# Performance work log

Hardware: AMD Instinct MI355X
Metric: run time of the kernel (lower is better)

Reference implementation:

```python
import jax, jax.numpy as jnp
import numpy as np

WINDOW = 7
NUM_HEADS = 12

def _relative_position_index(ws: int) -> np.ndarray:
    coords = np.stack(np.meshgrid(np.arange(ws), np.arange(ws), indexing='ij'))  # (2, ws, ws)
    flat = coords.reshape(2, -1)  # (2, N)
    rel = flat[:, :, None] - flat[:, None, :]  # (2, N, N)
    rel = rel.transpose(1, 2, 0).copy()
    rel[:, :, 0] += ws - 1
    rel[:, :, 1] += ws - 1
    rel[:, :, 0] *= 2 * ws - 1
    return rel.sum(-1)  # (N, N) int

REL_IDX = jnp.asarray(_relative_position_index(WINDOW))  # (49, 49)

def setup_inputs() -> dict:
    key = jax.random.key(0)
    ks = jax.random.split(key, 7)
    B_, N, C = 2048, 49, 384
    nW = 64
    return {
        'x': jax.random.normal(ks[0], (B_, N, C), jnp.float32),
        'mask': jax.random.normal(ks[1], (nW, N, N), jnp.float32),
        'qkv_w': jax.random.normal(ks[2], (3 * C, C), jnp.float32) * 0.02,
        'qkv_b': jax.random.normal(ks[3], (3 * C,), jnp.float32) * 0.02,
        'proj_w': jax.random.normal(ks[4], (C, C), jnp.float32) * 0.02,
        'proj_b': jax.random.normal(ks[5], (C,), jnp.float32) * 0.02,
        'rel_bias_table': jax.random.normal(ks[6], ((2 * WINDOW - 1) ** 2, NUM_HEADS), jnp.float32) * 0.02,
    }

def reference(x, mask, qkv_w, qkv_b, proj_w, proj_b, rel_bias_table):
    B_, N, C = x.shape
    H = NUM_HEADS
    D = C // H
    scale = D ** -0.5
    # fused qkv projection: (B_, N, 3C) -> (3, B_, H, N, D)
    qkv = (x @ qkv_w.T + qkv_b).reshape(B_, N, 3, H, D).transpose(2, 0, 3, 1, 4)
    q, k, v = qkv[0], qkv[1], qkv[2]
    attn = jnp.einsum('bhnd,bhmd->bhnm', q, k) * scale  # (B_, H, N, N)
    # relative position bias gather: (N, N, H) -> (H, N, N)
    bias = rel_bias_table[REL_IDX].transpose(2, 0, 1)
    attn = attn + bias[None]
    nW = mask.shape[0]
    B = B_ // nW
    attn = attn.reshape(B, nW, H, N, N) + mask[None, :, None]
    attn = attn.reshape(B_, H, N, N)
    attn = jax.nn.softmax(attn, axis=-1)
    out = jnp.einsum('bhnm,bhmd->bnhd', attn, v).reshape(B_, N, C)
    return out @ proj_w.T + proj_b
```

## Files before the change

kernel.cpp:

```cpp
#include <hip/hip_runtime.h>
#include <hip/hip_bf16.h>
#include <stdint.h>
#include <stddef.h>

typedef __attribute__((ext_vector_type(8))) short short8;
typedef __attribute__((ext_vector_type(4))) float floatx4;

#define GLDS16(gptr, lptr)                                                         \
  __builtin_amdgcn_global_load_lds(                                                \
      (const __attribute__((address_space(1))) void*)(gptr),                       \
      (__attribute__((address_space(3))) void*)(lptr), 16, 0, 0)

#define MTOT  100352
#define KDIM  384
#define NQKV  1152
#define NPROJ 384

__global__ void cvt_kernel(const float* __restrict__ in,
                           __hip_bfloat16* __restrict__ out, int n4) {
    int i = blockIdx.x * blockDim.x + threadIdx.x;
    if (i >= n4) return;
    float4 v = ((const float4*)in)[i];
    __hip_bfloat16* o = out + (size_t)i * 4;
    o[0] = __float2bfloat16(v.x);
    o[1] = __float2bfloat16(v.y);
    o[2] = __float2bfloat16(v.z);
    o[3] = __float2bfloat16(v.w);
}

__global__ void build_bias_kernel(const float* __restrict__ tbl,
                                  const float* __restrict__ mask,
                                  float* __restrict__ combined) {
    int tid = blockIdx.x * 256 + threadIdx.x;
    if (tid >= 12 * 64 * 2401) return;
    int hw = tid / 2401;
    int nm = tid - hw * 2401;
    int h  = hw / 64;
    int w2 = hw - h * 64;
    int n = nm / 49;
    int m = nm - n * 49;
    int i1 = n / 7, j1 = n - i1 * 7;
    int i2 = m / 7, j2 = m - i2 * 7;
    int ridx = (i1 - i2 + 6) * 13 + (j1 - j2 + 6);
    combined[tid] = tbl[ridx * 12 + h] + mask[(size_t)w2 * 2401 + nm];
}

template <int EPI>
__global__ __launch_bounds__(256) void gemm_bt_kernel(
    const __hip_bfloat16* __restrict__ A, const __hip_bfloat16* __restrict__ B,
    const float* __restrict__ bias, float* __restrict__ Cout,
    __hip_bfloat16* __restrict__ qbuf, __hip_bfloat16* __restrict__ kbuf,
    __hip_bfloat16* __restrict__ vbuf, int N) {
    __shared__ __hip_bfloat16 sA[128 * 32];
    __shared__ __hip_bfloat16 sB[128 * 32];
    const int t = threadIdx.x;
    const int bm = blockIdx.x, bn = blockIdx.y;
    const int lane = t & 63;
    const int w = t >> 6;
    const int wm = w & 1, wn = w >> 1;
    const int quad = lane >> 4, l15 = lane & 15;
    const int srow = t >> 2;
    const int scol = (t & 3) << 3;

    const __hip_bfloat16* Ab = A + (size_t)bm * 128 * KDIM;
    const __hip_bfloat16* Bb = B + (size_t)bn * 128 * KDIM;

    const floatx4 fzero = {0.f, 0.f, 0.f, 0.f};
    floatx4 acc[4][4];
#pragma unroll
    for (int i = 0; i < 4; ++i)
#pragma unroll
        for (int j = 0; j < 4; ++j) acc[i][j] = fzero;

    for (int kk = 0; kk < KDIM; kk += 32) {
        GLDS16(Ab + (size_t)srow * KDIM + kk + scol, &sA[srow * 32 + scol]);
        GLDS16(Ab + (size_t)(srow + 64) * KDIM + kk + scol,
               &sA[(srow + 64) * 32 + scol]);
        GLDS16(Bb + (size_t)srow * KDIM + kk + scol, &sB[srow * 32 + scol]);
        GLDS16(Bb + (size_t)(srow + 64) * KDIM + kk + scol,
               &sB[(srow + 64) * 32 + scol]);
        __syncthreads();
        short8 af[4], bf[4];
#pragma unroll
        for (int i = 0; i < 4; ++i)
            af[i] = *(const short8*)&sA[(wm * 64 + i * 16 + l15) * 32 + quad * 8];
#pragma unroll
        for (int j = 0; j < 4; ++j)
            bf[j] = *(const short8*)&sB[(wn * 64 + j * 16 + l15) * 32 + quad * 8];
#pragma unroll
        for (int i = 0; i < 4; ++i)
#pragma unroll
            for (int j = 0; j < 4; ++j)
                acc[i][j] = __builtin_amdgcn_mfma_f32_16x16x32_bf16(
                    af[i], bf[j], acc[i][j], 0, 0, 0);
        __syncthreads();
    }

    if (EPI == 0) {
        const float scale = 0.17677669529663687f;
#pragma unroll
        for (int j = 0; j < 4; ++j) {
            const int col = bn * 128 + wn * 64 + j * 16 + l15;
            const int part = col / 384;
            const int within = col - part * 384;
            const int hh = within >> 5;
            const int d = within & 31;
            __hip_bfloat16* dst = (part == 0) ? qbuf : ((part == 1) ? kbuf : vbuf);
            const float bv = bias[col];
            const float mul = (part == 0) ? scale : 1.0f;
#pragma unroll
            for (int i = 0; i < 4; ++i) {
#pragma unroll
                for (int r = 0; r < 4; ++r) {
                    const int row = bm * 128 + wm * 64 + i * 16 + quad * 4 + r;
                    const int b = row / 49;
                    const int nn = row - b * 49;
                    const float val = (acc[i][j][r] + bv) * mul;
                    dst[(((size_t)b * 12 + hh) * 49 + nn) * 32 + d] =
                        __float2bfloat16(val);
                }
            }
        }
    } else {
#pragma unroll
        for (int j = 0; j < 4; ++j) {
            const int col = bn * 128 + wn * 64 + j * 16 + l15;
            const float bv = bias[col];
#pragma unroll
            for (int i = 0; i < 4; ++i) {
#pragma unroll
                for (int r = 0; r < 4; ++r) {
                    const int row = bm * 128 + wm * 64 + i * 16 + quad * 4 + r;
                    Cout[(size_t)row * N + col] = acc[i][j][r] + bv;
                }
            }
        }
    }
}

__global__ __launch_bounds__(64) void attn_kernel(
    const __hip_bfloat16* __restrict__ qbuf,
    const __hip_bfloat16* __restrict__ kbuf,
    const __hip_bfloat16* __restrict__ vbuf,
    const float* __restrict__ combined,
    __hip_bfloat16* __restrict__ attn_out) {
    __shared__ __hip_bfloat16 sP[64 * 64];
    const int id = blockIdx.x;
    const int h = id % 12;
    const int b_ = id / 12;
    const int wdx = b_ & 63;
    const int lane = threadIdx.x;
    const int quad = lane >> 4, l15 = lane & 15;
    const size_t base = (size_t)(b_ * 12 + h) * (49 * 32);
    const short* qb = (const short*)qbuf + base;
    const short* kb = (const short*)kbuf + base;
    const short* vb = (const short*)vbuf + base;

    const floatx4 fzero = {0.f, 0.f, 0.f, 0.f};

    short8 aQ[4], bK[4];
#pragma unroll
    for (int i = 0; i < 4; ++i) {
        int r = i * 16 + l15;
        r = r > 48 ? 48 : r;
        aQ[i] = *(const short8*)(qb + r * 32 + quad * 8);
    }
#pragma unroll
    for (int j = 0; j < 4; ++j) {
        int n = j * 16 + l15;
        n = n > 48 ? 48 : n;
        bK[j] = *(const short8*)(kb + n * 32 + quad * 8);
    }

    floatx4 S[4][4];
#pragma unroll
    for (int i = 0; i < 4; ++i)
#pragma unroll
        for (int j = 0; j < 4; ++j)
            S[i][j] =
                __builtin_amdgcn_mfma_f32_16x16x32_bf16(aQ[i], bK[j], fzero, 0, 0, 0);

    const float* cb = combined + (size_t)(h * 64 + wdx) * 2401;
#pragma unroll
    for (int i = 0; i < 4; ++i) {
#pragma unroll
        for (int r = 0; r < 4; ++r) {
            const int row = i * 16 + quad * 4 + r;
            float v0[4];
#pragma unroll
            for (int j = 0; j < 4; ++j) {
                const int col = j * 16 + l15;
                float s = S[i][j][r];
                if (row < 49 && col < 49)
                    s += cb[row * 49 + col];
                else
                    s = -1e30f;
                v0[j] = s;
            }
            float mx = fmaxf(fmaxf(v0[0], v0[1]), fmaxf(v0[2], v0[3]));
#pragma unroll
            for (int off = 8; off > 0; off >>= 1) mx = fmaxf(mx, __shfl_xor(mx, off));
            float sum = 0.f;
#pragma unroll
            for (int j = 0; j < 4; ++j) {
                v0[j] = __expf(v0[j] - mx);
                sum += v0[j];
            }
#pragma unroll
            for (int off = 8; off > 0; off >>= 1) sum += __shfl_xor(sum, off);
            const float inv = 1.0f / sum;
#pragma unroll
            for (int j = 0; j < 4; ++j)
                sP[row * 64 + j * 16 + l15] = __float2bfloat16(v0[j] * inv);
        }
    }
    __syncthreads();

    short8 aP[4][2];
#pragma unroll
    for (int i = 0; i < 4; ++i)
#pragma unroll
        for (int kk = 0; kk < 2; ++kk)
            aP[i][kk] =
                *(const short8*)&sP[(i * 16 + l15) * 64 + kk * 32 + quad * 8];

    short8 bV[2][2];
#pragma unroll
    for (int jd = 0; jd < 2; ++jd)
#pragma unroll
        for (int kk = 0; kk < 2; ++kk) {
            short8 tmp;
#pragma unroll
            for (int jj = 0; jj < 8; ++jj) {
                int k = kk * 32 + quad * 8 + jj;
                k = k > 48 ? 48 : k;
                tmp[jj] = vb[k * 32 + jd * 16 + l15];
            }
            bV[jd][kk] = tmp;
        }

    floatx4 O[4][2];
#pragma unroll
    for (int i = 0; i < 4; ++i)
#pragma unroll
        for (int jd = 0; jd < 2; ++jd) {
            floatx4 o = __builtin_amdgcn_mfma_f32_16x16x32_bf16(aP[i][0], bV[jd][0],
                                                                fzero, 0, 0, 0);
            o = __builtin_amdgcn_mfma_f32_16x16x32_bf16(aP[i][1], bV[jd][1], o, 0, 0,
                                                        0);
            O[i][jd] = o;
        }

#pragma unroll
    for (int i = 0; i < 4; ++i) {
#pragma unroll
        for (int r = 0; r < 4; ++r) {
            const int row = i * 16 + quad * 4 + r;
            if (row < 49) {
#pragma unroll
                for (int jd = 0; jd < 2; ++jd) {
                    attn_out[((size_t)b_ * 49 + row) * 384 + h * 32 + jd * 16 + l15] =
                        __float2bfloat16(O[i][jd][r]);
                }
            }
        }
    }
}

extern "C" void kernel_launch(void* const* d_in, const int* in_sizes, int n_in,
                              void* d_out, int out_size, void* d_ws,
                              size_t ws_size, hipStream_t stream) {
    (void)in_sizes; (void)n_in; (void)out_size; (void)ws_size;
    const float* x      = (const float*)d_in[0];
    const float* mask   = (const float*)d_in[1];
    const float* qkv_w  = (const float*)d_in[2];
    const float* qkv_b  = (const float*)d_in[3];
    const float* proj_w = (const float*)d_in[4];
    const float* proj_b = (const float*)d_in[5];
    const float* tbl    = (const float*)d_in[6];
    float* out = (float*)d_out;
    char* ws = (char*)d_ws;

    __hip_bfloat16* x_bf    = (__hip_bfloat16*)(ws);
    __hip_bfloat16* wq_bf   = (__hip_bfloat16*)(ws + 77070336);
    __hip_bfloat16* wp_bf   = (__hip_bfloat16*)(ws + 77955072);
    float*          combined = (float*)(ws + 78249984);
    __hip_bfloat16* q_buf   = (__hip_bfloat16*)(ws + 85625856);
    __hip_bfloat16* k_buf   = (__hip_bfloat16*)(ws + 162696192);
    __hip_bfloat16* v_buf   = (__hip_bfloat16*)(ws + 239766528);
    __hip_bfloat16* attn_out = x_bf;

    cvt_kernel<<<(MTOT * KDIM / 4 + 255) / 256, 256, 0, stream>>>(x, x_bf,
                                                                  MTOT * KDIM / 4);
    cvt_kernel<<<(NQKV * KDIM / 4 + 255) / 256, 256, 0, stream>>>(
        qkv_w, wq_bf, NQKV * KDIM / 4);
    cvt_kernel<<<(NPROJ * KDIM / 4 + 255) / 256, 256, 0, stream>>>(
        proj_w, wp_bf, NPROJ * KDIM / 4);
    build_bias_kernel<<<(12 * 64 * 2401 + 255) / 256, 256, 0, stream>>>(tbl, mask,
                                                                        combined);
    gemm_bt_kernel<0><<<dim3(MTOT / 128, NQKV / 128), 256, 0, stream>>>(
        x_bf, wq_bf, qkv_b, nullptr, q_buf, k_buf, v_buf, NQKV);
    attn_kernel<<<2048 * 12, 64, 0, stream>>>(q_buf, k_buf, v_buf, combined,
                                              attn_out);
    gemm_bt_kernel<1><<<dim3(MTOT / 128, NPROJ / 128), 256, 0, stream>>>(
        attn_out, wp_bf, proj_b, out, nullptr, nullptr, nullptr, NPROJ);
}
```

Measured before the change: 657.8 us.

## Deepen GEMM K-tile with swizzled LDS, remap grid, transpose S and V layout in attention

The GEMM K-step grows from 32 to 64, LDS gets an XOR swizzle against bank conflicts, blocks are remapped into chunks of 16 M-tiles per N column for L2 reuse, and launch bounds request 4 blocks per CU. The attention kernel computes S transposed so each lane owns a row, reads a padded 52-wide bias with float4 loads, and cuts softmax shuffles to two per row. When the workspace is large enough, V is stored transposed so B fragments load as one vector instead of eight scalar gathers. Block order is changed to h-major, and the bias buffer now reuses the qkv weight region, so it is built after the QKV GEMM.

```diff
diff --git a/kernel.cpp b/kernel.cpp
--- a/kernel.cpp
+++ b/kernel.cpp
@@ -15,6 +15,11 @@
 #define KDIM  384
 #define NQKV  1152
 #define NPROJ 384
+
+static __device__ __forceinline__ unsigned short bfu(float f) {
+    __hip_bfloat16 h = __float2bfloat16(f);
+    return *(unsigned short*)&h;
+}
 
 __global__ void cvt_kernel(const float* __restrict__ in,
                            __hip_bfloat16* __restrict__ out, int n4) {
@@ -30,37 +35,48 @@
 
 __global__ void build_bias_kernel(const float* __restrict__ tbl,
                                   const float* __restrict__ mask,
-                                  float* __restrict__ combined) {
+                                  float* __restrict__ comb) {
     int tid = blockIdx.x * 256 + threadIdx.x;
-    if (tid >= 12 * 64 * 2401) return;
-    int hw = tid / 2401;
-    int nm = tid - hw * 2401;
-    int h  = hw / 64;
-    int w2 = hw - h * 64;
-    int n = nm / 49;
-    int m = nm - n * 49;
-    int i1 = n / 7, j1 = n - i1 * 7;
-    int i2 = m / 7, j2 = m - i2 * 7;
-    int ridx = (i1 - i2 + 6) * 13 + (j1 - j2 + 6);
-    combined[tid] = tbl[ridx * 12 + h] + mask[(size_t)w2 * 2401 + nm];
+    if (tid >= 12 * 64 * 49 * 52) return;
+    int hw = tid / 2548;
+    int nm = tid - hw * 2548;
+    int row = nm / 52;
+    int col = nm - row * 52;
+    int h = hw >> 6;
+    int w2 = hw & 63;
+    float v = -1e30f;
+    if (col < 49) {
+        int i1 = row / 7, j1 = row - i1 * 7;
+        int i2 = col / 7, j2 = col - i2 * 7;
+        int ridx = (i1 - i2 + 6) * 13 + (j1 - j2 + 6);
+        v = tbl[ridx * 12 + h] + mask[(size_t)w2 * 2401 + row * 49 + col];
+    }
+    comb[tid] = v;
 }
 
 template <int EPI>
-__global__ __launch_bounds__(256) void gemm_bt_kernel(
+__global__ __launch_bounds__(256, 4) void gemm_bt_kernel(
     const __hip_bfloat16* __restrict__ A, const __hip_bfloat16* __restrict__ B,
     const float* __restrict__ bias, float* __restrict__ Cout,
     __hip_bfloat16* __restrict__ qbuf, __hip_bfloat16* __restrict__ kbuf,
-    __hip_bfloat16* __restrict__ vbuf, int N) {
-    __shared__ __hip_bfloat16 sA[128 * 32];
-    __shared__ __hip_bfloat16 sB[128 * 32];
+    __hip_bfloat16* __restrict__ vbuf, int N, int NBN, int vt_mode) {
+    __shared__ __hip_bfloat16 sA[128 * 64];
+    __shared__ __hip_bfloat16 sB[128 * 64];
     const int t = threadIdx.x;
-    const int bm = blockIdx.x, bn = blockIdx.y;
+    const int per_chunk = 16 * NBN;
+    const int chunk = blockIdx.x / per_chunk;
+    const int rr = blockIdx.x - chunk * per_chunk;
+    const int bn = rr >> 4;
+    const int bm = chunk * 16 + (rr & 15);
+
     const int lane = t & 63;
     const int w = t >> 6;
     const int wm = w & 1, wn = w >> 1;
     const int quad = lane >> 4, l15 = lane & 15;
-    const int srow = t >> 2;
-    const int scol = (t & 3) << 3;
+    const int srow = t >> 3;
+    const int scg = t & 7;
+    const int sg = scg ^ (srow & 7);
+    const int rsw = l15 & 7;
 
     const __hip_bfloat16* Ab = A + (size_t)bm * 128 * KDIM;
     const __hip_bfloat16* Bb = B + (size_t)bn * 128 * KDIM;
@@ -72,196 +88,241 @@
 #pragma unroll
         for (int j = 0; j < 4; ++j) acc[i][j] = fzero;
 
-    for (int kk = 0; kk < KDIM; kk += 32) {
-        GLDS16(Ab + (size_t)srow * KDIM + kk + scol, &sA[srow * 32 + scol]);
-        GLDS16(Ab + (size_t)(srow + 64) * KDIM + kk + scol,
-               &sA[(srow + 64) * 32 + scol]);
-        GLDS16(Bb + (size_t)srow * KDIM + kk + scol, &sB[srow * 32 + scol]);
-        GLDS16(Bb + (size_t)(srow + 64) * KDIM + kk + scol,
-               &sB[(srow + 64) * 32 + scol]);
+    for (int kk = 0; kk < KDIM; kk += 64) {
+#pragma unroll
+        for (int i = 0; i < 4; ++i) {
+            const int r0 = srow + i * 32;
+            GLDS16(Ab + (size_t)r0 * KDIM + kk + sg * 8, &sA[r0 * 64 + scg * 8]);
+            GLDS16(Bb + (size_t)r0 * KDIM + kk + sg * 8, &sB[r0 * 64 + scg * 8]);
+        }
         __syncthreads();
-        short8 af[4], bf[4];
-#pragma unroll
-        for (int i = 0; i < 4; ++i)
-            af[i] = *(const short8*)&sA[(wm * 64 + i * 16 + l15) * 32 + quad * 8];
-#pragma unroll
-        for (int j = 0; j < 4; ++j)
-            bf[j] = *(const short8*)&sB[(wn * 64 + j * 16 + l15) * 32 + quad * 8];
-#pragma unroll
-        for (int i = 0; i < 4; ++i)
+#pragma unroll
+        for (int kk2 = 0; kk2 < 2; ++kk2) {
+            short8 af[4], bf[4];
+#pragma unroll
+            for (int i = 0; i < 4; ++i)
+                af[i] = *(const short8*)&sA[(wm * 64 + i * 16 + l15) * 64 +
+                                            ((kk2 * 4 + quad) ^ rsw) * 8];
 #pragma unroll
             for (int j = 0; j < 4; ++j)
-                acc[i][j] = __builtin_amdgcn_mfma_f32_16x16x32_bf16(
-                    af[i], bf[j], acc[i][j], 0, 0, 0);
+                bf[j] = *(const short8*)&sB[(wn * 64 + j * 16 + l15) * 64 +
+                                            ((kk2 * 4 + quad) ^ rsw) * 8];
+#pragma unroll
+            for (int i = 0; i < 4; ++i)
+#pragma unroll
+                for (int j = 0; j < 4; ++j)
+                    acc[i][j] = __builtin_amdgcn_mfma_f32_16x16x32_bf16(
+                        af[i], bf[j], acc[i][j], 0, 0, 0);
+        }
         __syncthreads();
+    }
+
+    int colv[4];
+    float bv4[4];
+#pragma unroll
+    for (int j = 0; j < 4; ++j) {
+        colv[j] = bn * 128 + wn * 64 + j * 16 + l15;
+        bv4[j] = bias[colv[j]];
     }
 
     if (EPI == 0) {
         const float scale = 0.17677669529663687f;
+        int partv[4], hv4[4], dv4[4];
 #pragma unroll
         for (int j = 0; j < 4; ++j) {
-            const int col = bn * 128 + wn * 64 + j * 16 + l15;
-            const int part = col / 384;
-            const int within = col - part * 384;
-            const int hh = within >> 5;
-            const int d = within & 31;
-            __hip_bfloat16* dst = (part == 0) ? qbuf : ((part == 1) ? kbuf : vbuf);
-            const float bv = bias[col];
-            const float mul = (part == 0) ? scale : 1.0f;
-#pragma unroll
-            for (int i = 0; i < 4; ++i) {
-#pragma unroll
-                for (int r = 0; r < 4; ++r) {
-                    const int row = bm * 128 + wm * 64 + i * 16 + quad * 4 + r;
-                    const int b = row / 49;
-                    const int nn = row - b * 49;
-                    const float val = (acc[i][j][r] + bv) * mul;
-                    dst[(((size_t)b * 12 + hh) * 49 + nn) * 32 + d] =
-                        __float2bfloat16(val);
+            partv[j] = colv[j] >= 768 ? 2 : (colv[j] >= 384 ? 1 : 0);
+            int within = colv[j] - partv[j] * 384;
+            hv4[j] = within >> 5;
+            dv4[j] = within & 31;
+        }
+#pragma unroll
+        for (int i = 0; i < 4; ++i) {
+#pragma unroll
+            for (int r = 0; r < 4; ++r) {
+                const int row = bm * 128 + wm * 64 + i * 16 + quad * 4 + r;
+                const int b = row / 49;
+                const int nn = row - b * 49;
+#pragma unroll
+                for (int j = 0; j < 4; ++j) {
+                    const float val = acc[i][j][r] + bv4[j];
+                    const size_t bh = (size_t)b * 12 + hv4[j];
+                    if (partv[j] == 0)
+                        qbuf[(bh * 49 + nn) * 32 + dv4[j]] =
+                            __float2bfloat16(val * scale);
+                    else if (partv[j] == 1)
+                        kbuf[(bh * 49 + nn) * 32 + dv4[j]] = __float2bfloat16(val);
+                    else {
+                        if (vt_mode)
+                            vbuf[(bh * 32 + dv4[j]) * 56 + nn] = __float2bfloat16(val);
+                        else
+                            vbuf[(bh * 49 + nn) * 32 + dv4[j]] = __float2bfloat16(val);
+                    }
                 }
             }
         }
     } else {
 #pragma unroll
-        for (int j = 0; j < 4; ++j) {
-            const int col = bn * 128 + wn * 64 + j * 16 + l15;
-            const float bv = bias[col];
-#pragma unroll
-            for (int i = 0; i < 4; ++i) {
-#pragma unroll
-                for (int r = 0; r < 4; ++r) {
-                    const int row = bm * 128 + wm * 64 + i * 16 + quad * 4 + r;
-                    Cout[(size_t)row * N + col] = acc[i][j][r] + bv;
-                }
-            }
-        }
-    }
-}
-
+        for (int i = 0; i < 4; ++i) {
+#pragma unroll
+            for (int r = 0; r < 4; ++r) {
+                const int row = bm * 128 + wm * 64 + i * 16 + quad * 4 + r;
+#pragma unroll
+                for (int j = 0; j < 4; ++j)
+                    Cout[(size_t)row * N + colv[j]] = acc[i][j][r] + bv4[j];
+            }
+        }
+    }
+}
+
+template <int VT>
 __global__ __launch_bounds__(64) void attn_kernel(
     const __hip_bfloat16* __restrict__ qbuf,
     const __hip_bfloat16* __restrict__ kbuf,
-    const __hip_bfloat16* __restrict__ vbuf,
-    const float* __restrict__ combined,
+    const __hip_bfloat16* __restrict__ vslab,
+    const float* __restrict__ comb,
     __hip_bfloat16* __restrict__ attn_out) {
-    __shared__ __hip_bfloat16 sP[64 * 64];
+    __shared__ unsigned short sP[64 * 72];
     const int id = blockIdx.x;
-    const int h = id % 12;
-    const int b_ = id / 12;
-    const int wdx = b_ & 63;
+    const int h = id >> 11;
+    const int rem = id & 2047;
+    const int w = rem >> 5;
+    const int b = rem & 31;
+    const int b_ = b * 64 + w;
     const int lane = threadIdx.x;
     const int quad = lane >> 4, l15 = lane & 15;
-    const size_t base = (size_t)(b_ * 12 + h) * (49 * 32);
-    const short* qb = (const short*)qbuf + base;
-    const short* kb = (const short*)kbuf + base;
-    const short* vb = (const short*)vbuf + base;
+    const size_t bh = (size_t)b_ * 12 + h;
+    const short* qb = (const short*)qbuf + bh * 1568;
+    const short* kb = (const short*)kbuf + bh * 1568;
+    const short* vb = (const short*)vslab + bh * (VT ? 1792 : 1568);
 
     const floatx4 fzero = {0.f, 0.f, 0.f, 0.f};
 
-    short8 aQ[4], bK[4];
-#pragma unroll
-    for (int i = 0; i < 4; ++i) {
-        int r = i * 16 + l15;
-        r = r > 48 ? 48 : r;
-        aQ[i] = *(const short8*)(qb + r * 32 + quad * 8);
-    }
-#pragma unroll
-    for (int j = 0; j < 4; ++j) {
-        int n = j * 16 + l15;
+    short8 bQ[4], aK[4];
+#pragma unroll
+    for (int im = 0; im < 4; ++im) {
+        int m = im * 16 + l15;
+        m = m > 48 ? 48 : m;
+        bQ[im] = *(const short8*)(qb + m * 32 + quad * 8);
+    }
+#pragma unroll
+    for (int jn = 0; jn < 4; ++jn) {
+        int n = jn * 16 + l15;
         n = n > 48 ? 48 : n;
-        bK[j] = *(const short8*)(kb + n * 32 + quad * 8);
-    }
-
-    floatx4 S[4][4];
-#pragma unroll
-    for (int i = 0; i < 4; ++i)
-#pragma unroll
-        for (int j = 0; j < 4; ++j)
-            S[i][j] =
-                __builtin_amdgcn_mfma_f32_16x16x32_bf16(aQ[i], bK[j], fzero, 0, 0, 0);
-
-    const float* cb = combined + (size_t)(h * 64 + wdx) * 2401;
-#pragma unroll
-    for (int i = 0; i < 4; ++i) {
+        aK[jn] = *(const short8*)(kb + n * 32 + quad * 8);
+    }
+
+    floatx4 ST[4][4];
+#pragma unroll
+    for (int im = 0; im < 4; ++im)
+#pragma unroll
+        for (int jn = 0; jn < 4; ++jn)
+            ST[im][jn] = __builtin_amdgcn_mfma_f32_16x16x32_bf16(aK[jn], bQ[im],
+                                                                 fzero, 0, 0, 0);
+
+    const float* cb = comb + (size_t)(h * 64 + w) * 2548;
+#pragma unroll
+    for (int im = 0; im < 4; ++im) {
+        const int m = im * 16 + l15;
+        const int mrow = m > 48 ? 48 : m;
+        const float* rp = cb + mrow * 52;
+        float v[16];
+#pragma unroll
+        for (int jn = 0; jn < 3; ++jn) {
+            float4 c4 = *(const float4*)(rp + jn * 16 + quad * 4);
+            v[jn * 4 + 0] = ST[im][jn][0] + c4.x;
+            v[jn * 4 + 1] = ST[im][jn][1] + c4.y;
+            v[jn * 4 + 2] = ST[im][jn][2] + c4.z;
+            v[jn * 4 + 3] = ST[im][jn][3] + c4.w;
+        }
+        {
+            const float s48 = rp[48];
+            v[12] = (quad == 0) ? (ST[im][3][0] + s48) : -1e30f;
+            v[13] = -1e30f;
+            v[14] = -1e30f;
+            v[15] = -1e30f;
+        }
+        float mx = v[0];
+#pragma unroll
+        for (int q = 1; q < 16; ++q) mx = fmaxf(mx, v[q]);
+        mx = fmaxf(mx, __shfl_xor(mx, 16));
+        mx = fmaxf(mx, __shfl_xor(mx, 32));
+        float sum = 0.f;
+#pragma unroll
+        for (int q = 0; q < 16; ++q) {
+            v[q] = __expf(v[q] - mx);
+            sum += v[q];
+        }
+        sum += __shfl_xor(sum, 16);
+        sum += __shfl_xor(sum, 32);
+        const float inv = 1.0f / sum;
+#pragma unroll
+        for (int jn = 0; jn < 4; ++jn) {
+            uint2 pk;
+            pk.x = (unsigned int)bfu(v[jn * 4 + 0] * inv) |
+                   ((unsigned int)bfu(v[jn * 4 + 1] * inv) << 16);
+            pk.y = (unsigned int)bfu(v[jn * 4 + 2] * inv) |
+                   ((unsigned int)bfu(v[jn * 4 + 3] * inv) << 16);
+            *(uint2*)&sP[m * 72 + jn * 16 + quad * 4] = pk;
+        }
+    }
+    __syncthreads();
+
+    short8 aP[4][2];
+#pragma unroll
+    for (int im = 0; im < 4; ++im)
+#pragma unroll
+        for (int kk = 0; kk < 2; ++kk)
+            aP[im][kk] =
+                *(const short8*)&sP[(im * 16 + l15) * 72 + kk * 32 + quad * 8];
+
+    short8 bV[2][2];
+    if (VT) {
+#pragma unroll
+        for (int jd = 0; jd < 2; ++jd)
+#pragma unroll
+            for (int kk = 0; kk < 2; ++kk) {
+                int n0 = kk * 32 + quad * 8;
+                n0 = n0 > 48 ? 48 : n0;
+                bV[jd][kk] = *(const short8*)(vb + (jd * 16 + l15) * 56 + n0);
+            }
+    } else {
+#pragma unroll
+        for (int jd = 0; jd < 2; ++jd)
+#pragma unroll
+            for (int kk = 0; kk < 2; ++kk) {
+                short8 tmp;
+#pragma unroll
+                for (int jj = 0; jj < 8; ++jj) {
+                    int k = kk * 32 + quad * 8 + jj;
+                    k = k > 48 ? 48 : k;
+                    tmp[jj] = vb[k * 32 + jd * 16 + l15];
+                }
+                bV[jd][kk] = tmp;
+            }
+    }
+
+    floatx4 O[4][2];
+#pragma unroll
+    for (int im = 0; im < 4; ++im)
+#pragma unroll
+        for (int jd = 0; jd < 2; ++jd) {
+            floatx4 o = __builtin_amdgcn_mfma_f32_16x16x32_bf16(aP[im][0], bV[jd][0],
+                                                                fzero, 0, 0, 0);
+            o = __builtin_amdgcn_mfma_f32_16x16x32_bf16(aP[im][1], bV[jd][1], o, 0,
+                                                        0, 0);
+            O[im][jd] = o;
+        }
+
+#pragma unroll
+    for (int im = 0; im < 4; ++im) {
 #pragma unroll
         for (int r = 0; r < 4; ++r) {
-            const int row = i * 16 + quad * 4 + r;
-            float v0[4];
-#pragma unroll
-            for (int j = 0; j < 4; ++j) {
-                const int col = j * 16 + l15;
-                float s = S[i][j][r];
-                if (row < 49 && col < 49)
-                    s += cb[row * 49 + col];
-                else
-                    s = -1e30f;
-                v0[j] = s;
-            }
-            float mx = fmaxf(fmaxf(v0[0], v0[1]), fmaxf(v0[2], v0[3]));
-#pragma unroll
-            for (int off = 8; off > 0; off >>= 1) mx = fmaxf(mx, __shfl_xor(mx, off));
-            float sum = 0.f;
-#pragma unroll
-            for (int j = 0; j < 4; ++j) {
-                v0[j] = __expf(v0[j] - mx);
-                sum += v0[j];
-            }
-#pragma unroll
-            for (int off = 8; off > 0; off >>= 1) sum += __shfl_xor(sum, off);
-            const float inv = 1.0f / sum;
-#pragma unroll
-            for (int j = 0; j < 4; ++j)
-                sP[row * 64 + j * 16 + l15] = __float2bfloat16(v0[j] * inv);
-        }
-    }
-    __syncthreads();
-
-    short8 aP[4][2];
-#pragma unroll
-    for (int i = 0; i < 4; ++i)
-#pragma unroll
-        for (int kk = 0; kk < 2; ++kk)
-            aP[i][kk] =
-                *(const short8*)&sP[(i * 16 + l15) * 64 + kk * 32 + quad * 8];
-
-    short8 bV[2][2];
-#pragma unroll
-    for (int jd = 0; jd < 2; ++jd)
-#pragma unroll
-        for (int kk = 0; kk < 2; ++kk) {
-            short8 tmp;
-#pragma unroll
-            for (int jj = 0; jj < 8; ++jj) {
-                int k = kk * 32 + quad * 8 + jj;
-                k = k > 48 ? 48 : k;
-                tmp[jj] = vb[k * 32 + jd * 16 + l15];
-            }
-            bV[jd][kk] = tmp;
-        }
-
-    floatx4 O[4][2];
-#pragma unroll
-    for (int i = 0; i < 4; ++i)
-#pragma unroll
-        for (int jd = 0; jd < 2; ++jd) {
-            floatx4 o = __builtin_amdgcn_mfma_f32_16x16x32_bf16(aP[i][0], bV[jd][0],
-                                                                fzero, 0, 0, 0);
-            o = __builtin_amdgcn_mfma_f32_16x16x32_bf16(aP[i][1], bV[jd][1], o, 0, 0,
-                                                        0);
-            O[i][jd] = o;
-        }
-
-#pragma unroll
-    for (int i = 0; i < 4; ++i) {
-#pragma unroll
-        for (int r = 0; r < 4; ++r) {
-            const int row = i * 16 + quad * 4 + r;
-            if (row < 49) {
-#pragma unroll
-                for (int jd = 0; jd < 2; ++jd) {
-                    attn_out[((size_t)b_ * 49 + row) * 384 + h * 32 + jd * 16 + l15] =
-                        __float2bfloat16(O[i][jd][r]);
-                }
+            const int m = im * 16 + quad * 4 + r;
+            if (m < 49) {
+#pragma unroll
+                for (int jd = 0; jd < 2; ++jd)
+                    attn_out[((size_t)b_ * 49 + m) * 384 + h * 32 + jd * 16 + l15] =
+                        __float2bfloat16(O[im][jd][r]);
             }
         }
     }
@@ -270,7 +331,7 @@
 extern "C" void kernel_launch(void* const* d_in, const int* in_sizes, int n_in,
                               void* d_out, int out_size, void* d_ws,
                               size_t ws_size, hipStream_t stream) {
-    (void)in_sizes; (void)n_in; (void)out_size; (void)ws_size;
+    (void)in_sizes; (void)n_in; (void)out_size;
     const float* x      = (const float*)d_in[0];
     const float* mask   = (const float*)d_in[1];
     const float* qkv_w  = (const float*)d_in[2];
@@ -281,14 +342,16 @@
     float* out = (float*)d_out;
     char* ws = (char*)d_ws;
 
-    __hip_bfloat16* x_bf    = (__hip_bfloat16*)(ws);
-    __hip_bfloat16* wq_bf   = (__hip_bfloat16*)(ws + 77070336);
-    __hip_bfloat16* wp_bf   = (__hip_bfloat16*)(ws + 77955072);
-    float*          combined = (float*)(ws + 78249984);
-    __hip_bfloat16* q_buf   = (__hip_bfloat16*)(ws + 85625856);
-    __hip_bfloat16* k_buf   = (__hip_bfloat16*)(ws + 162696192);
-    __hip_bfloat16* v_buf   = (__hip_bfloat16*)(ws + 239766528);
+    __hip_bfloat16* x_bf  = (__hip_bfloat16*)(ws);
+    __hip_bfloat16* wq_bf = (__hip_bfloat16*)(ws + 77070336);
+    float*          comb  = (float*)(ws + 77070336);
+    __hip_bfloat16* wp_bf = (__hip_bfloat16*)(ws + 84897792);
+    __hip_bfloat16* q_buf = (__hip_bfloat16*)(ws + 85192704);
+    __hip_bfloat16* k_buf = (__hip_bfloat16*)(ws + 162263040);
+    __hip_bfloat16* v_slab = (__hip_bfloat16*)(ws + 239333376);
     __hip_bfloat16* attn_out = x_bf;
+
+    const int vt = (ws_size >= (size_t)327413760) ? 1 : 0;
 
     cvt_kernel<<<(MTOT * KDIM / 4 + 255) / 256, 256, 0, stream>>>(x, x_bf,
                                                                   MTOT * KDIM / 4);
@@ -296,12 +359,18 @@
         qkv_w, wq_bf, NQKV * KDIM / 4);
     cvt_kernel<<<(NPROJ * KDIM / 4 + 255) / 256, 256, 0, stream>>>(
         proj_w, wp_bf, NPROJ * KDIM / 4);
-    build_bias_kernel<<<(12 * 64 * 2401 + 255) / 256, 256, 0, stream>>>(tbl, mask,
-                                                                        combined);
-    gemm_bt_kernel<0><<<dim3(MTOT / 128, NQKV / 128), 256, 0, stream>>>(
-        x_bf, wq_bf, qkv_b, nullptr, q_buf, k_buf, v_buf, NQKV);
-    attn_kernel<<<2048 * 12, 64, 0, stream>>>(q_buf, k_buf, v_buf, combined,
-                                              attn_out);
-    gemm_bt_kernel<1><<<dim3(MTOT / 128, NPROJ / 128), 256, 0, stream>>>(
-        attn_out, wp_bf, proj_b, out, nullptr, nullptr, nullptr, NPROJ);
-}
+    gemm_bt_kernel<0><<<784 * 9, 256, 0, stream>>>(x_bf, wq_bf, qkv_b, nullptr,
+                                                   q_buf, k_buf, v_slab, NQKV, 9,
+                                                   vt);
+    build_bias_kernel<<<(12 * 64 * 49 * 52 + 255) / 256, 256, 0, stream>>>(
+        tbl, mask, comb);
+    if (vt)
+        attn_kernel<1><<<2048 * 12, 64, 0, stream>>>(q_buf, k_buf, v_slab, comb,
+                                                     attn_out);
+    else
+        attn_kernel<0><<<2048 * 12, 64, 0, stream>>>(q_buf, k_buf, v_slab, comb,
+                                                     attn_out);
+    gemm_bt_kernel<1><<<784 * 3, 256, 0, stream>>>(attn_out, wp_bf, proj_b, out,
+                                                   nullptr, nullptr, nullptr,
+                                                   NPROJ, 3, 0);
+}
```

After: 612.5 us. 1.07x faster.
